# Kernel tuning notes

Hardware: AMD Instinct MI355X
Metric: run time of the kernel (lower is better)

Reference implementation:

```python
import jax, jax.numpy as jnp
import numpy as np

B = 512       # number of graphs
MAX_N = 128   # pad length (>= max(num_atoms))
D = 256       # emb_dim


def setup_inputs() -> dict:
    key = jax.random.key(0)
    ks = jax.random.split(key, 20)
    num_atoms_np = np.full(B, 80, dtype=np.int64)
    num_atoms_np[: B // 2] = 112
    num_atoms_np[B // 2 :] = 48
    total = int(num_atoms_np.sum())  # 40960, static
    scale = 1.0 / np.sqrt(D)

    def lin_w(k):
        return jax.random.normal(k, (D, D), jnp.float32) * scale

    inp = {
        'rep_2d': jax.random.normal(ks[0], (total, D), jnp.float32),
        'rep_3d': jax.random.normal(ks[1], (total, D), jnp.float32),
        'num_atoms': jnp.asarray(num_atoms_np),
        # mha_2d_3d (queries from 2d, keys/values from 3d)
        'wq23': lin_w(ks[2]), 'bq23': jnp.zeros((D,), jnp.float32),
        'wk23': lin_w(ks[3]), 'bk23': jnp.zeros((D,), jnp.float32),
        'wv23': lin_w(ks[4]), 'bv23': jnp.zeros((D,), jnp.float32),
        # mha_3d_2d (queries from 3d, keys/values from 2d)
        'wq32': lin_w(ks[5]), 'bq32': jnp.zeros((D,), jnp.float32),
        'wk32': lin_w(ks[6]), 'bk32': jnp.zeros((D,), jnp.float32),
        'wv32': lin_w(ks[7]), 'bv32': jnp.zeros((D,), jnp.float32),
        # per-branch Linear (normalizer=Identity) + GELU
        'wm23': lin_w(ks[8]), 'bm23': jnp.zeros((D,), jnp.float32),
        'wm32': lin_w(ks[9]), 'bm32': jnp.zeros((D,), jnp.float32),
    }
    return inp


def _variadic_to_padded(flat, num_atoms):
    # flat: [total, D] -> padded [B, MAX_N, D], mask [B, MAX_N] (True = valid)
    cum = jnp.cumsum(num_atoms)
    offsets = cum - num_atoms
    pos = jnp.arange(MAX_N)
    mask = pos[None, :] < num_atoms[:, None]
    idx = jnp.where(mask, offsets[:, None] + pos[None, :], 0)
    padded = flat[idx] * mask[..., None].astype(flat.dtype)
    return padded, mask


def _padded_to_variadic(padded, num_atoms, total):
    # padded: [B, MAX_N, D] -> flat [total, D]
    cum = jnp.cumsum(num_atoms)
    t = jnp.arange(total)
    b = jnp.searchsorted(cum, t, side='right')
    i = t - (cum - num_atoms)[b]
    return padded[b, i]


def _cross_attn(q_in, kv_in, mask, wq, bq, wk, bk, wv, bv):
    # single-head scaled dot-product cross-attention, key-side padding mask
    q = q_in @ wq.T + bq
    k = kv_in @ wk.T + bk
    v = kv_in @ wv.T + bv
    s = jnp.einsum('bqd,bkd->bqk', q, k) / jnp.sqrt(jnp.asarray(D, q.dtype))
    s = jnp.where(mask[:, None, :], s, jnp.asarray(-1e9, s.dtype))
    a = jax.nn.softmax(s, axis=-1)
    return jnp.einsum('bqk,bkd->bqd', a, v)


def reference(rep_2d, rep_3d, num_atoms,
              wq23, bq23, wk23, bk23, wv23, bv23,
              wq32, bq32, wk32, bk32, wv32, bv32,
              wm23, bm23, wm32, bm32):
    total = rep_2d.shape[0]
    p2d, mask = _variadic_to_padded(rep_2d, num_atoms)
    p3d, _ = _variadic_to_padded(rep_3d, num_atoms)
    x2d = _cross_attn(p2d, p3d, mask, wq23, bq23, wk23, bk23, wv23, bv23)
    x3d = _cross_attn(p3d, p2d, mask, wq32, bq32, wk32, bk32, wv32, bv32)
    x2d = _padded_to_variadic(x2d, num_atoms, total)
    x3d = _padded_to_variadic(x3d, num_atoms, total)
    out2d = jax.nn.gelu(x2d @ wm23.T + bm23, approximate=False)
    out3d = jax.nn.gelu(x3d @ wm32.T + bm32, approximate=False)
    return (out2d, out3d)
```

## Files before the change

### kernel.cpp

```cpp
#include <hip/hip_runtime.h>
#include <hip/hip_bf16.h>
#include <cstdint>


typedef short s16x8 __attribute__((ext_vector_type(8)));
typedef float f32x4 __attribute__((ext_vector_type(4)));

__device__ __forceinline__ s16x8 cvt8(const float* p) {
  float4 a0 = *(const float4*)p, a1 = *(const float4*)(p + 4);
  union { s16x8 v; __bf16 e[8]; } u;
  u.e[0] = (__bf16)a0.x; u.e[1] = (__bf16)a0.y; u.e[2] = (__bf16)a0.z; u.e[3] = (__bf16)a0.w;
  u.e[4] = (__bf16)a1.x; u.e[5] = (__bf16)a1.y; u.e[6] = (__bf16)a1.z; u.e[7] = (__bf16)a1.w;
  return u.v;
}
__device__ __forceinline__ float fast_gelu(float x) {
  float ax = fabsf(x);
  float t = 1.0f / (1.0f + 0.3275911f * (ax * 0.70710678f));
  float y = t * (0.254829592f + t * (-0.284496736f + t * (1.421413741f +
            t * (-1.453152027f + t * 1.061405429f))));
  float er = 1.0f - y * __expf(-0.5f * ax * ax);
  er = (x < 0.f) ? -er : er;
  return 0.5f * x * (1.0f + er);
}

__global__ void sentinel_kernel(float* out, float v) {
  if (threadIdx.x == 0 && blockIdx.x == 0) out[0] = v;
}

__global__ __launch_bounds__(512) void scan_kernel(
    const int* __restrict__ na, int* __restrict__ offs, int* __restrict__ perm,
    int B, int total, float* out)
{
  __shared__ int s32[512];
  __shared__ int s64[512];
  __shared__ uint4 sv[512];
  const int t = threadIdx.x;
  int v32 = 0, v64 = 0;
  if (t < B) {
    v32 = na[t];
    v64 = (int)((const long long*)na)[t];
  }
  s32[t] = v32; s64[t] = v64;
  __syncthreads();
  for (int o = 1; o < 512; o <<= 1) {
    int a = (t >= o) ? s32[t - o] : 0;
    int b = (t >= o) ? s64[t - o] : 0;
    __syncthreads();
    s32[t] += a; s64[t] += b;
    __syncthreads();
  }
  int tot32 = s32[B - 1], tot64 = s64[B - 1];
  bool ok32 = (tot32 == total), ok64 = (tot64 == total);
  int offv = ok32 ? (s32[t] - v32) : ok64 ? (s64[t] - v64) : 0;
  if (t < B) offs[t] = offv;
  if (t == 0) {
    offs[B] = ok32 ? tot32 : ok64 ? tot64 : 0;
    if (!ok32 && !ok64) out[0] = 31337.0f;
  }
  __syncthreads();

  const int key = (offv >> 7) & 7;
  uint4 oh = (uint4){0, 0, 0, 0};
  if (t < B) ((unsigned*)&oh)[key >> 1] = 1u << ((key & 1) * 16);
  sv[t] = oh;
  __syncthreads();
  for (int o = 1; o < 512; o <<= 1) {
    uint4 a = (t >= o) ? sv[t - o] : (uint4){0, 0, 0, 0};
    __syncthreads();
    sv[t].x += a.x; sv[t].y += a.y; sv[t].z += a.z; sv[t].w += a.w;
    __syncthreads();
  }
  uint4 totv = sv[B - 1];
  int count[8], cap[8];
  #pragma unroll
  for (int k = 0; k < 8; ++k) {
    count[k] = (((unsigned*)&totv)[k >> 1] >> ((k & 1) * 16)) & 0xFFFF;
    cap[k] = (k < B) ? ((B - 1 - k) / 8 + 1) : 0;
  }
  int rank = ((((unsigned*)&sv[t])[key >> 1] >> ((key & 1) * 16)) & 0xFFFF) - 1;
  bool lo = false;
  if (t < B) {
    if (rank < cap[key]) perm[key + 8 * rank] = t;
    else lo = true;
  }
  __syncthreads();
  s32[t] = lo ? 1 : 0;
  __syncthreads();
  for (int o = 1; o < 512; o <<= 1) {
    int a = (t >= o) ? s32[t - o] : 0;
    __syncthreads();
    s32[t] += a;
    __syncthreads();
  }
  if (lo) {
    int lr = s32[t] - 1;
    int used[8], eb = 0, k = 0, j = 0;
    #pragma unroll
    for (int q = 0; q < 8; ++q) used[q] = (count[q] < cap[q]) ? count[q] : cap[q];
    #pragma unroll
    for (int q = 0; q < 8; ++q) {
      int freeq = cap[q] - used[q];
      if (lr >= eb && lr < eb + freeq) { k = q; j = used[q] + (lr - eb); }
      eb += freeq;
    }
    perm[k + 8 * j] = t;
  }
}

__global__ __launch_bounds__(256) void cvt2_kernel(
    const float* __restrict__ in0, const float* __restrict__ in1,
    __bf16* __restrict__ out0, __bf16* __restrict__ out1) {
  const float* in = blockIdx.y ? in1 : in0;
  __bf16* out = blockIdx.y ? out1 : out0;
  int i = (blockIdx.x * 256 + threadIdx.x) * 4;
  float4 f = *(const float4*)(in + i);
  out[i + 0] = (__bf16)f.x; out[i + 1] = (__bf16)f.y;
  out[i + 2] = (__bf16)f.z; out[i + 3] = (__bf16)f.w;
}

__global__ __launch_bounds__(256) void gemm_kernel(
    const float* __restrict__ A, const float* __restrict__ Bw,
    const float* __restrict__ bias, __bf16* __restrict__ C, int N)
{
  __shared__ __bf16 At[128 * 32];
  __shared__ __bf16 Bt[128 * 32];
  const int t = threadIdx.x;
  const int lane = t & 63, w = t >> 6;
  const int wr = w >> 1, wc = w & 1;
  const int l15 = lane & 15, l4 = lane >> 4;
  const int by = blockIdx.x, bx = blockIdx.y;

  f32x4 acc[4][4];
  for (int m = 0; m < 4; ++m)
    for (int nn = 0; nn < 4; ++nn) acc[m][nn] = (f32x4){0.f, 0.f, 0.f, 0.f};

  for (int kk = 0; kk < 256; kk += 32) {
    for (int j = 0; j < 2; ++j) {
      int c = t + j * 256;
      int row = c >> 2, off0 = (c & 3) * 8;
      *(s16x8*)(&At[row * 32 + off0]) = cvt8(A + (size_t)(by * 128 + row) * 256 + kk + off0);
      *(s16x8*)(&Bt[row * 32 + off0]) = cvt8(Bw + (size_t)(bx * 128 + row) * 256 + kk + off0);
    }
    __syncthreads();
    s16x8 af[4], bfr[4];
    for (int m = 0; m < 4; ++m)
      af[m] = *(const s16x8*)(&At[(wr * 64 + m * 16 + l15) * 32 + l4 * 8]);
    for (int nn = 0; nn < 4; ++nn)
      bfr[nn] = *(const s16x8*)(&Bt[(wc * 64 + nn * 16 + l15) * 32 + l4 * 8]);
    for (int m = 0; m < 4; ++m)
      for (int nn = 0; nn < 4; ++nn)
        acc[m][nn] = __builtin_amdgcn_mfma_f32_16x16x32_bf16(af[m], bfr[nn], acc[m][nn], 0, 0, 0);
    __syncthreads();
  }

  for (int m = 0; m < 4; ++m) {
    int row0 = by * 128 + wr * 64 + m * 16 + l4 * 4;
    for (int nn = 0; nn < 4; ++nn) {
      int col = bx * 128 + wc * 64 + nn * 16 + l15;
      float bc = bias[col];
      for (int r = 0; r < 4; ++r) {
        int row = row0 + r;
        C[(size_t)row * N + col] = (__bf16)(acc[m][nn][r] + bc);
      }
    }
  }
}

#define CTP 136
__global__ __launch_bounds__(256) void vgemm_kernel(
    const float* __restrict__ A, const float* __restrict__ Bw,
    const float* __restrict__ bias, __bf16* __restrict__ Vt, int total)
{
  __shared__ __bf16 At[128 * 32];
  __shared__ __bf16 Bt[128 * 32];
  __shared__ __bf16 Ct[128 * CTP];
  const int t = threadIdx.x;
  const int lane = t & 63, w = t >> 6;
  const int wr = w >> 1, wc = w & 1;
  const int l15 = lane & 15, l4 = lane >> 4;
  const int by = blockIdx.y;
  const int bx = blockIdx.x;

  f32x4 acc[4][4];
  for (int m = 0; m < 4; ++m)
    for (int nn = 0; nn < 4; ++nn) acc[m][nn] = (f32x4){0.f, 0.f, 0.f, 0.f};

  for (int kk = 0; kk < 256; kk += 32) {
    for (int j = 0; j < 2; ++j) {
      int c = t + j * 256;
      int row = c >> 2, off0 = (c & 3) * 8;
      *(s16x8*)(&At[row * 32 + off0]) = cvt8(A + (size_t)(by * 128 + row) * 256 + kk + off0);
      *(s16x8*)(&Bt[row * 32 + off0]) = cvt8(Bw + (size_t)(bx * 128 + row) * 256 + kk + off0);
    }
    __syncthreads();
    s16x8 af[4], bfr[4];
    for (int m = 0; m < 4; ++m)
      af[m] = *(const s16x8*)(&At[(wr * 64 + m * 16 + l15) * 32 + l4 * 8]);
    for (int nn = 0; nn < 4; ++nn)
      bfr[nn] = *(const s16x8*)(&Bt[(wc * 64 + nn * 16 + l15) * 32 + l4 * 8]);
    for (int m = 0; m < 4; ++m)
      for (int nn = 0; nn < 4; ++nn)
        acc[m][nn] = __builtin_amdgcn_mfma_f32_16x16x32_bf16(af[m], bfr[nn], acc[m][nn], 0, 0, 0);
    __syncthreads();
  }

  for (int m = 0; m < 4; ++m) {
    int rl0 = wr * 64 + m * 16 + l4 * 4;
    for (int nn = 0; nn < 4; ++nn) {
      int cl = wc * 64 + nn * 16 + l15;
      for (int r = 0; r < 4; ++r) {
        int rl = rl0 + r;
        Ct[rl * CTP + cl] = (__bf16)(acc[m][nn][r] + bias[by * 128 + rl]);
      }
    }
  }
  __syncthreads();

  for (int i = 0; i < 8; ++i) {
    int c = t + i * 256;
    int tile = c >> 5, w5 = c & 31;
    int kb_l = tile >> 3, db_l = tile & 7;
    int d_l = w5 & 15, kh = w5 >> 4;
    *(uint4*)(Vt + (((size_t)(bx * 8 + kb_l) * 16 + (by * 8 + db_l)) << 8) + w5 * 8) =
        *(const uint4*)(&Ct[(db_l * 16 + d_l) * CTP + kb_l * 16 + kh * 8]);
  }
}

struct Attn2Args {
  const __bf16* Q[2]; const __bf16* K[2]; const __bf16* V[2];
  unsigned long long X[2];
};
#define KP 264
#define PP 136
#define XP 272
__global__ __launch_bounds__(512, 2) void attn2_kernel(
    Attn2Args args, const int* __restrict__ offs, const int* __restrict__ perm,
    int total)
{
  __shared__ __bf16 smem[128 * 136];
  __bf16 (*Klds)[KP] = (__bf16(*)[KP])smem;
  __bf16 (*Plds)[PP] = (__bf16(*)[PP])smem;
  __bf16 (*XT)[XP]   = (__bf16(*)[XP])smem;

  const int br = blockIdx.y;
  const __bf16* Q  = args.Q[br];
  const __bf16* Km = args.K[br];
  const __bf16* Vt = args.V[br];
  __bf16* X = (__bf16*)args.X[br];

  const int g = perm[blockIdx.x];
  const int off = offs[g];
  const int n = offs[g + 1] - off;
  const int t = threadIdx.x, lane = t & 63, w = t >> 6;
  const int l15 = lane & 15, l4 = lane >> 4;
  const bool qact = (w * 16) < n;
  const bool big = (n > 64);

  const int srow = t >> 5, scol = (t & 31) * 16;
  uint4 kst[4];
  #pragma unroll
  for (int j = 0; j < 4; ++j)
    kst[j] = *(const uint4*)((const char*)(Km + (size_t)(off + j * 16 + srow) * 256) + scol);
  s16x8 qf[8];
  if (qact) {
    int qr = w * 16 + l15; if (qr >= n) qr = n - 1;
    const __bf16* qp = Q + (size_t)(off + qr) * 256 + l4 * 8;
    #pragma unroll
    for (int kk = 0; kk < 8; ++kk) qf[kk] = *(const s16x8*)(qp + kk * 32);
  }
  #pragma unroll
  for (int j = 0; j < 4; ++j)
    *(uint4*)((char*)&Klds[j * 16 + srow][0] + scol) = kst[j];
  uint4 kst1[4];
  if (big) {
    #pragma unroll
    for (int j = 0; j < 4; ++j)
      kst1[j] = *(const uint4*)((const char*)(Km + (size_t)(off + 64 + j * 16 + srow) * 256) + scol);
  }
  __syncthreads();

  f32x4 sacc[8];
  #pragma unroll
  for (int i = 0; i < 8; ++i) sacc[i] = (f32x4){0.f, 0.f, 0.f, 0.f};
  if (qact) {
    #pragma unroll
    for (int kt = 0; kt < 4; ++kt) {
      const __bf16* kp = &Klds[kt * 16 + l15][l4 * 8];
      #pragma unroll
      for (int kk = 0; kk < 8; ++kk) {
        s16x8 kf = *(const s16x8*)(kp + kk * 32);
        sacc[kt] = __builtin_amdgcn_mfma_f32_16x16x32_bf16(qf[kk], kf, sacc[kt], 0, 0, 0);
      }
    }
  }
  __syncthreads();
  if (big) {
    #pragma unroll
    for (int j = 0; j < 4; ++j)
      *(uint4*)((char*)&Klds[j * 16 + srow][0] + scol) = kst1[j];
    __syncthreads();
    if (qact) {
      #pragma unroll
      for (int kt = 0; kt < 4; ++kt) {
        const __bf16* kp = &Klds[kt * 16 + l15][l4 * 8];
        #pragma unroll
        for (int kk = 0; kk < 8; ++kk) {
          s16x8 kf = *(const s16x8*)(kp + kk * 32);
          sacc[4 + kt] = __builtin_amdgcn_mfma_f32_16x16x32_bf16(qf[kk], kf, sacc[4 + kt], 0, 0, 0);
        }
      }
    }
    __syncthreads();
  }

  if (qact) {
    #pragma unroll
    for (int r = 0; r < 4; ++r) {
      float sv[8];
      float m = -1e30f;
      #pragma unroll
      for (int kt = 0; kt < 8; ++kt) {
        int key = kt * 16 + l15;
        float v = (key < n) ? sacc[kt][r] * 0.0625f : -1e30f;
        sv[kt] = v; m = fmaxf(m, v);
      }
      for (int o = 1; o < 16; o <<= 1) m = fmaxf(m, __shfl_xor(m, o));
      float p[8], sum = 0.f;
      #pragma unroll
      for (int kt = 0; kt < 8; ++kt) { p[kt] = __expf(sv[kt] - m); sum += p[kt]; }
      for (int o = 1; o < 16; o <<= 1) sum += __shfl_xor(sum, o);
      float inv = 1.f / sum;
      int q = w * 16 + l4 * 4 + r;
      #pragma unroll
      for (int kt = 0; kt < 4; ++kt)
        Plds[q][kt * 16 + l15] = (__bf16)(p[kt] * inv);
      if (big) {
        #pragma unroll
        for (int kt = 4; kt < 8; ++kt)
          Plds[q][kt * 16 + l15] = (__bf16)(p[kt] * inv);
      }
    }
  }
  __syncthreads();

  const int dbase = w * 32;
  const int ktiles = total >> 4;
  f32x4 xacc[2][8];
  #pragma unroll
  for (int dt = 0; dt < 2; ++dt)
    #pragma unroll
    for (int qm = 0; qm < 8; ++qm) xacc[dt][qm] = (f32x4){0.f, 0.f, 0.f, 0.f};

  #pragma unroll
  for (int dt = 0; dt < 2; ++dt) {
    int db = w * 2 + dt;
    s16x8 vf[4];
    #pragma unroll
    for (int ks = 0; ks < 4; ++ks) {
      int kb = (off >> 4) + ks * 2 + (l4 >> 1);
      if (kb >= ktiles) kb = ktiles - 1;
      vf[ks] = *(const s16x8*)(Vt + (((size_t)kb * 16 + db) << 8)
                               + (l15 + ((l4 & 1) << 4)) * 8);
    }
    #pragma unroll
    for (int qm = 0; qm < 8; ++qm) {
      #pragma unroll
      for (int ks = 0; ks < 4; ++ks) {
        if (ks * 32 < n) {
          s16x8 pa = *(const s16x8*)(&Plds[qm * 16 + l15][ks * 32 + l4 * 8]);
          xacc[dt][qm] = __builtin_amdgcn_mfma_f32_16x16x32_bf16(pa, vf[ks], xacc[dt][qm], 0, 0, 0);
        }
      }
    }
  }
  __syncthreads();

  #pragma unroll
  for (int dt = 0; dt < 2; ++dt)
    #pragma unroll
    for (int qm = 0; qm < 4; ++qm)
      #pragma unroll
      for (int r = 0; r < 4; ++r)
        XT[qm * 16 + l4 * 4 + r][dbase + dt * 16 + l15] = (__bf16)xacc[dt][qm][r];
  __syncthreads();
  #pragma unroll
  for (int i = 0; i < 4; ++i) {
    int c = t + i * 512;
    int row = c >> 5, seg = c & 31;
    if (row < n)
      *(uint4*)(X + (size_t)(off + row) * 256 + seg * 8) =
          *(const uint4*)(&XT[row][seg * 8]);
  }
  if (big) {
    __syncthreads();
    #pragma unroll
    for (int dt = 0; dt < 2; ++dt)
      #pragma unroll
      for (int qm = 4; qm < 8; ++qm)
        #pragma unroll
        for (int r = 0; r < 4; ++r)
          XT[(qm - 4) * 16 + l4 * 4 + r][dbase + dt * 16 + l15] = (__bf16)xacc[dt][qm][r];
    __syncthreads();
    #pragma unroll
    for (int i = 0; i < 4; ++i) {
      int c = t + i * 512;
      int row = c >> 5, seg = c & 31;
      int grow = 64 + row;
      if (grow < n)
        *(uint4*)(X + (size_t)(off + grow) * 256 + seg * 8) =
            *(const uint4*)(&XT[row][seg * 8]);
    }
  }
}

#define OP 88
__global__ __launch_bounds__(256) void gemm_out(
    const __bf16* __restrict__ A, const __bf16* __restrict__ W,
    const float* __restrict__ bias, float* __restrict__ C, int swz)
{
  __shared__ __bf16 At[64 * OP];
  __shared__ __bf16 Bt[128 * OP];
  const int t = threadIdx.x;
  const int lane = t & 63, w = t >> 6;
  const int wr = w >> 1, wc = w & 1;
  const int l15 = lane & 15, l4 = lane >> 4;
  int b = blockIdx.x, by;
  if (swz) {
    int k = b & 7, q = b >> 3;
    by = ((k + ((q >> 1) << 3)) << 1) | (q & 1);
  } else by = b;
  const int bx = blockIdx.y;

  f32x4 acc[2][4];
  for (int m = 0; m < 2; ++m)
    for (int nn = 0; nn < 4; ++nn) acc[m][nn] = (f32x4){0.f, 0.f, 0.f, 0.f};

  for (int kk = 0; kk < 256; kk += 64) {
    #pragma unroll
    for (int j = 0; j < 2; ++j) {
      int c = t + j * 256;
      int row = c >> 3, off0 = (c & 7) * 8;
      *(s16x8*)(&At[row * OP + off0]) =
          *(const s16x8*)(A + (size_t)(by * 64 + row) * 256 + kk + off0);
    }
    #pragma unroll
    for (int j = 0; j < 4; ++j) {
      int c = t + j * 256;
      int row = c >> 3, off0 = (c & 7) * 8;
      *(s16x8*)(&Bt[row * OP + off0]) =
          *(const s16x8*)(W + (size_t)(bx * 128 + row) * 256 + kk + off0);
    }
    __syncthreads();
    #pragma unroll
    for (int k2 = 0; k2 < 2; ++k2) {
      s16x8 af[2], bfr[4];
      #pragma unroll
      for (int m = 0; m < 2; ++m)
        af[m] = *(const s16x8*)(&At[(wr * 32 + m * 16 + l15) * OP + k2 * 32 + l4 * 8]);
      #pragma unroll
      for (int nn = 0; nn < 4; ++nn)
        bfr[nn] = *(const s16x8*)(&Bt[(wc * 64 + nn * 16 + l15) * OP + k2 * 32 + l4 * 8]);
      #pragma unroll
      for (int m = 0; m < 2; ++m)
        #pragma unroll
        for (int nn = 0; nn < 4; ++nn)
          acc[m][nn] = __builtin_amdgcn_mfma_f32_16x16x32_bf16(af[m], bfr[nn], acc[m][nn], 0, 0, 0);
    }
    __syncthreads();
  }

  for (int m = 0; m < 2; ++m) {
    int row0 = by * 64 + wr * 32 + m * 16 + l4 * 4;
    for (int nn = 0; nn < 4; ++nn) {
      int col = bx * 128 + wc * 64 + nn * 16 + l15;
      float bc = bias[col];
      for (int r = 0; r < 4; ++r) {
        int row = row0 + r;
        C[(size_t)row * 256 + col] = fast_gelu(acc[m][nn][r] + bc);
      }
    }
  }
}

extern "C" void kernel_launch(void* const* d_in, const int* in_sizes, int n_in,
                              void* d_out, int out_size, void* d_ws, size_t ws_size,
                              hipStream_t stream) {
  const float* rep2d = (const float*)d_in[0];
  const float* rep3d = (const float*)d_in[1];
  const int*   na    = (const int*)d_in[2];
  const float* wq23 = (const float*)d_in[3];  const float* bq23 = (const float*)d_in[4];
  const float* wk23 = (const float*)d_in[5];  const float* bk23 = (const float*)d_in[6];
  const float* wv23 = (const float*)d_in[7];  const float* bv23 = (const float*)d_in[8];
  const float* wq32 = (const float*)d_in[9];  const float* bq32 = (const float*)d_in[10];
  const float* wk32 = (const float*)d_in[11]; const float* bk32 = (const float*)d_in[12];
  const float* wv32 = (const float*)d_in[13]; const float* bv32 = (const float*)d_in[14];
  const float* wm23 = (const float*)d_in[15]; const float* bm23 = (const float*)d_in[16];
  const float* wm32 = (const float*)d_in[17]; const float* bm32 = (const float*)d_in[18];

  const int B = in_sizes[2];
  const int total = in_sizes[0] / 256;
  float* out = (float*)d_out;

  char* ws = (char*)d_ws;
  const size_t SZ = (size_t)total * 256 * sizeof(__bf16);
  const size_t WMB = 65536 * sizeof(__bf16);
  const size_t need6 = 8192 + 2 * WMB + 6 * SZ;
  const size_t need3 = 8192 + 2 * WMB + 3 * SZ;
  int* offs = (int*)ws;
  int* perm = (int*)(ws + 4096);

  dim3 blk(256);
  dim3 blkA(512);
  dim3 gP(total / 128, 2);
  dim3 gV(total / 128, 2);
  dim3 gO(total / 64, 2);
  const int swz = ((total / 64) % 16 == 0) ? 1 : 0;

  if (ws_size >= need6) {
    __bf16* WM0 = (__bf16*)(ws + 8192);
    __bf16* WM1 = (__bf16*)(ws + 8192 + WMB);
    __bf16* BQ1 = (__bf16*)(ws + 8192 + 2 * WMB);
    __bf16* BK1 = (__bf16*)(ws + 8192 + 2 * WMB + SZ);
    __bf16* BV1 = (__bf16*)(ws + 8192 + 2 * WMB + 2 * SZ);
    __bf16* BQ2 = (__bf16*)(ws + 8192 + 2 * WMB + 3 * SZ);
    __bf16* BK2 = (__bf16*)(ws + 8192 + 2 * WMB + 4 * SZ);
    __bf16* BV2 = (__bf16*)(ws + 8192 + 2 * WMB + 5 * SZ);

    scan_kernel<<<1, 512, 0, stream>>>(na, offs, perm, B, total, out);
    cvt2_kernel<<<dim3(64, 2), blk, 0, stream>>>(wm23, wm32, WM0, WM1);
    gemm_kernel<<<gP, blk, 0, stream>>>(rep2d, wq23, bq23, BQ1, 256);
    gemm_kernel<<<gP, blk, 0, stream>>>(rep3d, wk23, bk23, BK1, 256);
    vgemm_kernel<<<gV, blk, 0, stream>>>(wv23, rep3d, bv23, BV1, total);
    gemm_kernel<<<gP, blk, 0, stream>>>(rep3d, wq32, bq32, BQ2, 256);
    gemm_kernel<<<gP, blk, 0, stream>>>(rep2d, wk32, bk32, BK2, 256);
    vgemm_kernel<<<gV, blk, 0, stream>>>(wv32, rep2d, bv32, BV2, total);

    Attn2Args aa;
    aa.Q[0] = BQ1; aa.K[0] = BK1; aa.V[0] = BV1; aa.X[0] = (unsigned long long)BQ1;
    aa.Q[1] = BQ2; aa.K[1] = BK2; aa.V[1] = BV2; aa.X[1] = (unsigned long long)BQ2;
    attn2_kernel<<<dim3(B, 2), blkA, 0, stream>>>(aa, offs, perm, total);

    gemm_out<<<gO, blk, 0, stream>>>(BQ1, WM0, bm23, out, swz);
    gemm_out<<<gO, blk, 0, stream>>>(BQ2, WM1, bm32, out + (size_t)total * 256, swz);
  } else if (ws_size >= need3) {
    __bf16* WM0 = (__bf16*)(ws + 8192);
    __bf16* WM1 = (__bf16*)(ws + 8192 + WMB);
    __bf16* BQ = (__bf16*)(ws + 8192 + 2 * WMB);
    __bf16* BK = (__bf16*)(ws + 8192 + 2 * WMB + SZ);
    __bf16* BV = (__bf16*)(ws + 8192 + 2 * WMB + 2 * SZ);

    scan_kernel<<<1, 512, 0, stream>>>(na, offs, perm, B, total, out);
    cvt2_kernel<<<dim3(64, 2), blk, 0, stream>>>(wm23, wm32, WM0, WM1);
    for (int br = 0; br < 2; ++br) {
      const float* rq = br ? rep3d : rep2d;
      const float* rk = br ? rep2d : rep3d;
      const float* wq = br ? wq32 : wq23;  const float* bq = br ? bq32 : bq23;
      const float* wk = br ? wk32 : wk23;  const float* bk = br ? bk32 : bk23;
      const float* wv = br ? wv32 : wv23;  const float* bv = br ? bv32 : bv23;
      __bf16* wm = br ? WM1 : WM0;         const float* bm = br ? bm32 : bm23;
      float* o = out + (size_t)br * total * 256;

      gemm_kernel<<<gP, blk, 0, stream>>>(rq, wq, bq, BQ, 256);
      gemm_kernel<<<gP, blk, 0, stream>>>(rk, wk, bk, BK, 256);
      vgemm_kernel<<<gV, blk, 0, stream>>>(wv, rk, bv, BV, total);
      Attn2Args aa;
      aa.Q[0] = BQ; aa.K[0] = BK; aa.V[0] = BV; aa.X[0] = (unsigned long long)BQ;
      aa.Q[1] = BQ; aa.K[1] = BK; aa.V[1] = BV; aa.X[1] = (unsigned long long)BQ;
      attn2_kernel<<<dim3(B, 1), blkA, 0, stream>>>(aa, offs, perm, total);
      gemm_out<<<gO, blk, 0, stream>>>(BQ, wm, bm, o, swz);
    }
  } else {
    sentinel_kernel<<<1, 64, 0, stream>>>(out, 54321.0f);
  }
}
```

Baseline: 205.8 us.

## Fold output projection into value weights and apply GELU in attention epilogue

Because softmax rows sum to one, the output Linear is applied to the value projection up front: Wc = Wm·Wv and bc = Wm·bv + bm are computed by two small new kernels. The V-GEMM then uses the combined bf16 weight, and the attention kernel writes GELU of its result straight to the fp32 output. This removes the two output GEMM launches and the bf16 round trip of the attention result through global memory. In exchange it adds two tiny weight-prep kernels, an extra bf16 rounding of the combined weight, and uncoalesced scattered fp32 stores from the attention epilogue in place of the LDS-staged store.

```diff
diff --git a/kernel.cpp b/kernel.cpp
--- a/kernel.cpp
+++ b/kernel.cpp
@@ -107,15 +107,101 @@
   }
 }
 
-__global__ __launch_bounds__(256) void cvt2_kernel(
-    const float* __restrict__ in0, const float* __restrict__ in1,
-    __bf16* __restrict__ out0, __bf16* __restrict__ out1) {
-  const float* in = blockIdx.y ? in1 : in0;
-  __bf16* out = blockIdx.y ? out1 : out0;
-  int i = (blockIdx.x * 256 + threadIdx.x) * 4;
-  float4 f = *(const float4*)(in + i);
-  out[i + 0] = (__bf16)f.x; out[i + 1] = (__bf16)f.y;
-  out[i + 2] = (__bf16)f.z; out[i + 3] = (__bf16)f.w;
+__global__ __launch_bounds__(256) void wc_kernel(
+    const float* __restrict__ Wm0, const float* __restrict__ Wv0,
+    const float* __restrict__ Wm1, const float* __restrict__ Wv1,
+    __bf16* __restrict__ Wcb0, __bf16* __restrict__ Wcb1)
+{
+  const int br = blockIdx.y;
+  const float* Wm = br ? Wm1 : Wm0;
+  const float* Wv = br ? Wv1 : Wv0;
+  __bf16* Wcb = br ? Wcb1 : Wcb0;
+  const int rt = blockIdx.x >> 1, ct = blockIdx.x & 1;
+  __shared__ __bf16 Am[128][40];
+  __shared__ __bf16 Bv[128][40];
+  const int t = threadIdx.x, lane = t & 63, w = t >> 6;
+  const int wr = w >> 1, wc = w & 1;
+  const int l15 = lane & 15, l4 = lane >> 4;
+
+  f32x4 acc[4][4];
+  for (int m = 0; m < 4; ++m)
+    for (int nn = 0; nn < 4; ++nn) acc[m][nn] = (f32x4){0.f, 0.f, 0.f, 0.f};
+
+  for (int kk = 0; kk < 256; kk += 32) {
+    #pragma unroll
+    for (int j = 0; j < 2; ++j) {
+      int c = t + j * 256;
+      int row = c >> 2, o0 = (c & 3) * 8;
+      *(s16x8*)(&Am[row][o0]) = cvt8(Wm + (size_t)(rt * 128 + row) * 256 + kk + o0);
+    }
+    #pragma unroll
+    for (int j = 0; j < 4; ++j) {
+      int c = t + j * 256;
+      int k = c >> 5, j4 = (c & 31) * 4;
+      float4 v = *(const float4*)(Wv + (size_t)(kk + k) * 256 + ct * 128 + j4);
+      Bv[j4 + 0][k] = (__bf16)v.x; Bv[j4 + 1][k] = (__bf16)v.y;
+      Bv[j4 + 2][k] = (__bf16)v.z; Bv[j4 + 3][k] = (__bf16)v.w;
+    }
+    __syncthreads();
+    s16x8 af[4], bfr[4];
+    #pragma unroll
+    for (int m = 0; m < 4; ++m)
+      af[m] = *(const s16x8*)(&Am[wr * 64 + m * 16 + l15][l4 * 8]);
+    #pragma unroll
+    for (int nn = 0; nn < 4; ++nn)
+      bfr[nn] = *(const s16x8*)(&Bv[wc * 64 + nn * 16 + l15][l4 * 8]);
+    #pragma unroll
+    for (int m = 0; m < 4; ++m)
+      #pragma unroll
+      for (int nn = 0; nn < 4; ++nn)
+        acc[m][nn] = __builtin_amdgcn_mfma_f32_16x16x32_bf16(af[m], bfr[nn], acc[m][nn], 0, 0, 0);
+    __syncthreads();
+  }
+
+  for (int m = 0; m < 4; ++m) {
+    int row0 = rt * 128 + wr * 64 + m * 16 + l4 * 4;
+    for (int nn = 0; nn < 4; ++nn) {
+      int col = ct * 128 + wc * 64 + nn * 16 + l15;
+      for (int r = 0; r < 4; ++r)
+        Wcb[(size_t)(row0 + r) * 256 + col] = (__bf16)acc[m][nn][r];
+    }
+  }
+}
+
+__global__ __launch_bounds__(256) void bc_kernel(
+    const float* __restrict__ Wm0, const float* __restrict__ bv0,
+    const float* __restrict__ bm0,
+    const float* __restrict__ Wm1, const float* __restrict__ bv1,
+    const float* __restrict__ bm1,
+    float* __restrict__ bc0, float* __restrict__ bc1)
+{
+  const int br = blockIdx.x;
+  const float* Wm = br ? Wm1 : Wm0;
+  const float* bv = br ? bv1 : bv0;
+  const float* bm = br ? bm1 : bm0;
+  float* bc = br ? bc1 : bc0;
+  __shared__ float bvl[256];
+  const int t = threadIdx.x, lane = t & 63, w = t >> 6;
+  bvl[t] = bv[t];
+  __syncthreads();
+  float b0 = bvl[lane * 4], b1 = bvl[lane * 4 + 1];
+  float b2 = bvl[lane * 4 + 2], b3 = bvl[lane * 4 + 3];
+  for (int i0 = 0; i0 < 64; i0 += 8) {
+    float part[8];
+    #pragma unroll
+    for (int i = 0; i < 8; ++i) {
+      int row = w * 64 + i0 + i;
+      float4 a = *(const float4*)(Wm + (size_t)row * 256 + lane * 4);
+      part[i] = a.x * b0 + a.y * b1 + a.z * b2 + a.w * b3;
+    }
+    #pragma unroll
+    for (int i = 0; i < 8; ++i) {
+      float s = part[i];
+      for (int o = 1; o < 64; o <<= 1) s += __shfl_xor(s, o);
+      int row = w * 64 + i0 + i;
+      if (lane == 0) bc[row] = s + bm[row];
+    }
+  }
 }
 
 __global__ __launch_bounds__(256) void gemm_kernel(
@@ -167,8 +253,8 @@
 }
 
 #define CTP 136
-__global__ __launch_bounds__(256) void vgemm_kernel(
-    const float* __restrict__ A, const float* __restrict__ Bw,
+__global__ __launch_bounds__(256) void vgemmB_kernel(
+    const __bf16* __restrict__ Ab, const float* __restrict__ Bw,
     const float* __restrict__ bias, __bf16* __restrict__ Vt, int total)
 {
   __shared__ __bf16 At[128 * 32];
@@ -189,7 +275,8 @@
     for (int j = 0; j < 2; ++j) {
       int c = t + j * 256;
       int row = c >> 2, off0 = (c & 3) * 8;
-      *(s16x8*)(&At[row * 32 + off0]) = cvt8(A + (size_t)(by * 128 + row) * 256 + kk + off0);
+      *(s16x8*)(&At[row * 32 + off0]) =
+          *(const s16x8*)(Ab + (size_t)(by * 128 + row) * 256 + kk + off0);
       *(s16x8*)(&Bt[row * 32 + off0]) = cvt8(Bw + (size_t)(bx * 128 + row) * 256 + kk + off0);
     }
     __syncthreads();
@@ -228,11 +315,10 @@
 
 struct Attn2Args {
   const __bf16* Q[2]; const __bf16* K[2]; const __bf16* V[2];
-  unsigned long long X[2];
+  unsigned long long O[2];
 };
 #define KP 264
 #define PP 136
-#define XP 272
 __global__ __launch_bounds__(512, 2) void attn2_kernel(
     Attn2Args args, const int* __restrict__ offs, const int* __restrict__ perm,
     int total)
@@ -240,13 +326,12 @@
   __shared__ __bf16 smem[128 * 136];
   __bf16 (*Klds)[KP] = (__bf16(*)[KP])smem;
   __bf16 (*Plds)[PP] = (__bf16(*)[PP])smem;
-  __bf16 (*XT)[XP]   = (__bf16(*)[XP])smem;
 
   const int br = blockIdx.y;
   const __bf16* Q  = args.Q[br];
   const __bf16* Km = args.K[br];
   const __bf16* Vt = args.V[br];
-  __bf16* X = (__bf16*)args.X[br];
+  float* Out = (float*)args.O[br];
 
   const int g = perm[blockIdx.x];
   const int off = offs[g];
@@ -373,112 +458,18 @@
       }
     }
   }
-  __syncthreads();
-
-  #pragma unroll
-  for (int dt = 0; dt < 2; ++dt)
-    #pragma unroll
-    for (int qm = 0; qm < 4; ++qm)
-      #pragma unroll
-      for (int r = 0; r < 4; ++r)
-        XT[qm * 16 + l4 * 4 + r][dbase + dt * 16 + l15] = (__bf16)xacc[dt][qm][r];
-  __syncthreads();
-  #pragma unroll
-  for (int i = 0; i < 4; ++i) {
-    int c = t + i * 512;
-    int row = c >> 5, seg = c & 31;
-    if (row < n)
-      *(uint4*)(X + (size_t)(off + row) * 256 + seg * 8) =
-          *(const uint4*)(&XT[row][seg * 8]);
-  }
-  if (big) {
-    __syncthreads();
-    #pragma unroll
-    for (int dt = 0; dt < 2; ++dt)
-      #pragma unroll
-      for (int qm = 4; qm < 8; ++qm)
-        #pragma unroll
-        for (int r = 0; r < 4; ++r)
-          XT[(qm - 4) * 16 + l4 * 4 + r][dbase + dt * 16 + l15] = (__bf16)xacc[dt][qm][r];
-    __syncthreads();
-    #pragma unroll
-    for (int i = 0; i < 4; ++i) {
-      int c = t + i * 512;
-      int row = c >> 5, seg = c & 31;
-      int grow = 64 + row;
-      if (grow < n)
-        *(uint4*)(X + (size_t)(off + grow) * 256 + seg * 8) =
-            *(const uint4*)(&XT[row][seg * 8]);
-    }
-  }
-}
-
-#define OP 88
-__global__ __launch_bounds__(256) void gemm_out(
-    const __bf16* __restrict__ A, const __bf16* __restrict__ W,
-    const float* __restrict__ bias, float* __restrict__ C, int swz)
-{
-  __shared__ __bf16 At[64 * OP];
-  __shared__ __bf16 Bt[128 * OP];
-  const int t = threadIdx.x;
-  const int lane = t & 63, w = t >> 6;
-  const int wr = w >> 1, wc = w & 1;
-  const int l15 = lane & 15, l4 = lane >> 4;
-  int b = blockIdx.x, by;
-  if (swz) {
-    int k = b & 7, q = b >> 3;
-    by = ((k + ((q >> 1) << 3)) << 1) | (q & 1);
-  } else by = b;
-  const int bx = blockIdx.y;
-
-  f32x4 acc[2][4];
-  for (int m = 0; m < 2; ++m)
-    for (int nn = 0; nn < 4; ++nn) acc[m][nn] = (f32x4){0.f, 0.f, 0.f, 0.f};
-
-  for (int kk = 0; kk < 256; kk += 64) {
-    #pragma unroll
-    for (int j = 0; j < 2; ++j) {
-      int c = t + j * 256;
-      int row = c >> 3, off0 = (c & 7) * 8;
-      *(s16x8*)(&At[row * OP + off0]) =
-          *(const s16x8*)(A + (size_t)(by * 64 + row) * 256 + kk + off0);
-    }
-    #pragma unroll
-    for (int j = 0; j < 4; ++j) {
-      int c = t + j * 256;
-      int row = c >> 3, off0 = (c & 7) * 8;
-      *(s16x8*)(&Bt[row * OP + off0]) =
-          *(const s16x8*)(W + (size_t)(bx * 128 + row) * 256 + kk + off0);
-    }
-    __syncthreads();
-    #pragma unroll
-    for (int k2 = 0; k2 < 2; ++k2) {
-      s16x8 af[2], bfr[4];
-      #pragma unroll
-      for (int m = 0; m < 2; ++m)
-        af[m] = *(const s16x8*)(&At[(wr * 32 + m * 16 + l15) * OP + k2 * 32 + l4 * 8]);
-      #pragma unroll
-      for (int nn = 0; nn < 4; ++nn)
-        bfr[nn] = *(const s16x8*)(&Bt[(wc * 64 + nn * 16 + l15) * OP + k2 * 32 + l4 * 8]);
-      #pragma unroll
-      for (int m = 0; m < 2; ++m)
-        #pragma unroll
-        for (int nn = 0; nn < 4; ++nn)
-          acc[m][nn] = __builtin_amdgcn_mfma_f32_16x16x32_bf16(af[m], bfr[nn], acc[m][nn], 0, 0, 0);
-    }
-    __syncthreads();
-  }
-
-  for (int m = 0; m < 2; ++m) {
-    int row0 = by * 64 + wr * 32 + m * 16 + l4 * 4;
-    for (int nn = 0; nn < 4; ++nn) {
-      int col = bx * 128 + wc * 64 + nn * 16 + l15;
-      float bc = bias[col];
+
+  #pragma unroll
+  for (int dt = 0; dt < 2; ++dt) {
+    int d = dbase + dt * 16 + l15;
+    #pragma unroll
+    for (int qm = 0; qm < 8; ++qm)
+      #pragma unroll
       for (int r = 0; r < 4; ++r) {
-        int row = row0 + r;
-        C[(size_t)row * 256 + col] = fast_gelu(acc[m][nn][r] + bc);
-      }
-    }
+        int q = qm * 16 + l4 * 4 + r;
+        if (q < n)
+          Out[(size_t)(off + q) * 256 + d] = fast_gelu(xacc[dt][qm][r]);
+      }
   }
 }
 
@@ -507,18 +498,18 @@
   const size_t need6 = 8192 + 2 * WMB + 6 * SZ;
   const size_t need3 = 8192 + 2 * WMB + 3 * SZ;
   int* offs = (int*)ws;
-  int* perm = (int*)(ws + 4096);
+  int* perm = (int*)(ws + 2560);
+  float* bc0 = (float*)(ws + 5120);
+  float* bc1 = (float*)(ws + 6144);
 
   dim3 blk(256);
   dim3 blkA(512);
   dim3 gP(total / 128, 2);
   dim3 gV(total / 128, 2);
-  dim3 gO(total / 64, 2);
-  const int swz = ((total / 64) % 16 == 0) ? 1 : 0;
 
   if (ws_size >= need6) {
-    __bf16* WM0 = (__bf16*)(ws + 8192);
-    __bf16* WM1 = (__bf16*)(ws + 8192 + WMB);
+    __bf16* WC0 = (__bf16*)(ws + 8192);
+    __bf16* WC1 = (__bf16*)(ws + 8192 + WMB);
     __bf16* BQ1 = (__bf16*)(ws + 8192 + 2 * WMB);
     __bf16* BK1 = (__bf16*)(ws + 8192 + 2 * WMB + SZ);
     __bf16* BV1 = (__bf16*)(ws + 8192 + 2 * WMB + 2 * SZ);
@@ -527,47 +518,45 @@
     __bf16* BV2 = (__bf16*)(ws + 8192 + 2 * WMB + 5 * SZ);
 
     scan_kernel<<<1, 512, 0, stream>>>(na, offs, perm, B, total, out);
-    cvt2_kernel<<<dim3(64, 2), blk, 0, stream>>>(wm23, wm32, WM0, WM1);
+    wc_kernel<<<dim3(4, 2), blk, 0, stream>>>(wm23, wv23, wm32, wv32, WC0, WC1);
+    bc_kernel<<<2, blk, 0, stream>>>(wm23, bv23, bm23, wm32, bv32, bm32, bc0, bc1);
     gemm_kernel<<<gP, blk, 0, stream>>>(rep2d, wq23, bq23, BQ1, 256);
     gemm_kernel<<<gP, blk, 0, stream>>>(rep3d, wk23, bk23, BK1, 256);
-    vgemm_kernel<<<gV, blk, 0, stream>>>(wv23, rep3d, bv23, BV1, total);
+    vgemmB_kernel<<<gV, blk, 0, stream>>>(WC0, rep3d, bc0, BV1, total);
     gemm_kernel<<<gP, blk, 0, stream>>>(rep3d, wq32, bq32, BQ2, 256);
     gemm_kernel<<<gP, blk, 0, stream>>>(rep2d, wk32, bk32, BK2, 256);
-    vgemm_kernel<<<gV, blk, 0, stream>>>(wv32, rep2d, bv32, BV2, total);
+    vgemmB_kernel<<<gV, blk, 0, stream>>>(WC1, rep2d, bc1, BV2, total);
 
     Attn2Args aa;
-    aa.Q[0] = BQ1; aa.K[0] = BK1; aa.V[0] = BV1; aa.X[0] = (unsigned long long)BQ1;
-    aa.Q[1] = BQ2; aa.K[1] = BK2; aa.V[1] = BV2; aa.X[1] = (unsigned long long)BQ2;
+    aa.Q[0] = BQ1; aa.K[0] = BK1; aa.V[0] = BV1; aa.O[0] = (unsigned long long)out;
+    aa.Q[1] = BQ2; aa.K[1] = BK2; aa.V[1] = BV2;
+    aa.O[1] = (unsigned long long)(out + (size_t)total * 256);
     attn2_kernel<<<dim3(B, 2), blkA, 0, stream>>>(aa, offs, perm, total);
-
-    gemm_out<<<gO, blk, 0, stream>>>(BQ1, WM0, bm23, out, swz);
-    gemm_out<<<gO, blk, 0, stream>>>(BQ2, WM1, bm32, out + (size_t)total * 256, swz);
   } else if (ws_size >= need3) {
-    __bf16* WM0 = (__bf16*)(ws + 8192);
-    __bf16* WM1 = (__bf16*)(ws + 8192 + WMB);
+    __bf16* WC0 = (__bf16*)(ws + 8192);
+    __bf16* WC1 = (__bf16*)(ws + 8192 + WMB);
     __bf16* BQ = (__bf16*)(ws + 8192 + 2 * WMB);
     __bf16* BK = (__bf16*)(ws + 8192 + 2 * WMB + SZ);
     __bf16* BV = (__bf16*)(ws + 8192 + 2 * WMB + 2 * SZ);
 
     scan_kernel<<<1, 512, 0, stream>>>(na, offs, perm, B, total, out);
-    cvt2_kernel<<<dim3(64, 2), blk, 0, stream>>>(wm23, wm32, WM0, WM1);
+    wc_kernel<<<dim3(4, 2), blk, 0, stream>>>(wm23, wv23, wm32, wv32, WC0, WC1);
+    bc_kernel<<<2, blk, 0, stream>>>(wm23, bv23, bm23, wm32, bv32, bm32, bc0, bc1);
     for (int br = 0; br < 2; ++br) {
       const float* rq = br ? rep3d : rep2d;
       const float* rk = br ? rep2d : rep3d;
       const float* wq = br ? wq32 : wq23;  const float* bq = br ? bq32 : bq23;
       const float* wk = br ? wk32 : wk23;  const float* bk = br ? bk32 : bk23;
-      const float* wv = br ? wv32 : wv23;  const float* bv = br ? bv32 : bv23;
-      __bf16* wm = br ? WM1 : WM0;         const float* bm = br ? bm32 : bm23;
+      __bf16* wcb = br ? WC1 : WC0;        float* bcv = br ? bc1 : bc0;
       float* o = out + (size_t)br * total * 256;
 
       gemm_kernel<<<gP, blk, 0, stream>>>(rq, wq, bq, BQ, 256);
       gemm_kernel<<<gP, blk, 0, stream>>>(rk, wk, bk, BK, 256);
-      vgemm_kernel<<<gV, blk, 0, stream>>>(wv, rk, bv, BV, total);
+      vgemmB_kernel<<<gV, blk, 0, stream>>>(wcb, rk, bcv, BV, total);
       Attn2Args aa;
-      aa.Q[0] = BQ; aa.K[0] = BK; aa.V[0] = BV; aa.X[0] = (unsigned long long)BQ;
-      aa.Q[1] = BQ; aa.K[1] = BK; aa.V[1] = BV; aa.X[1] = (unsigned long long)BQ;
+      aa.Q[0] = BQ; aa.K[0] = BK; aa.V[0] = BV; aa.O[0] = (unsigned long long)o;
+      aa.Q[1] = BQ; aa.K[1] = BK; aa.V[1] = BV; aa.O[1] = (unsigned long long)o;
       attn2_kernel<<<dim3(B, 1), blkA, 0, stream>>>(aa, offs, perm, total);
-      gemm_out<<<gO, blk, 0, stream>>>(BQ, wm, bm, o, swz);
     }
   } else {
     sentinel_kernel<<<1, 64, 0, stream>>>(out, 54321.0f);
```

New measurement: 223.4 us. 8.5% more time.
